# Kernel optimization log

Measured on AMD Instinct MI355X. Metric: run time of the kernel, lower is better.

The kernel has to match this reference:

```python
import jax, jax.numpy as jnp
import numpy as np

B, IN_C, OUT_C, NUM, DIM = 4096, 512, 512, 16, 128

def _unif(k, shape, fan_in):
    b = 1.0 / np.sqrt(fan_in)
    return jax.random.uniform(k, shape, jnp.float32, -b, b)

def setup_inputs() -> dict:
    key = jax.random.key(0)
    ks = jax.random.split(key, 9)
    inp = jax.random.normal(ks[0], (B, IN_C), jnp.float32)
    Wpre = _unif(ks[1], (DIM, IN_C), IN_C)        # nn.Linear weight (out, in)
    bpre = _unif(ks[2], (DIM,), IN_C)
    W = _unif(ks[3], (NUM, NUM, DIM, DIM), DIM)    # W[i,j] = link[i][j].weight (out=e, in=d)
    bl = _unif(ks[4], (NUM, NUM, DIM), DIM)        # link biases
    life = jax.random.uniform(ks[5], (NUM, NUM), jnp.float32) + 0.5  # rand(1)+0.5
    Wpost = _unif(ks[6], (OUT_C, DIM), DIM)
    bpost = _unif(ks[7], (OUT_C,), DIM)
    return {"inp": inp, "Wpre": Wpre, "bpre": bpre, "W": W, "b": bl,
            "life": life, "Wpost": Wpost, "bpost": bpost, "steps": 10}

def reference(inp, Wpre, bpre, W, b, life, Wpost, bpost, steps):
    num = life.shape[0]
    x = inp @ Wpre.T + bpre                         # [B, dim]
    gate = jnp.where(life > 0, life, 0.0)           # life>0 branch with scalar gain
    Wg = gate[:, :, None, None] * W                 # [num, num, dim, dim]
    bias = jnp.einsum('ij,ijd->jd', gate, b)        # per-step constant bias sum over i
    m0 = jnp.zeros((num,) + x.shape, x.dtype).at[0].set(x)  # matrix[0] = inp
    def step(m, _):
        # new[j] = sum_i gate[i,j] * (m[i] @ W[i,j].T + b[i,j])
        new = jnp.einsum('ibd,ijed->jbe', m, Wg) + bias[:, None, :]
        return new, None
    mT, _ = jax.lax.scan(step, m0, None, length=steps)
    return mT[num - 1] @ Wpost.T + bpost            # [B, out_c]
```

## Files before the change

kernel.cpp:

```cpp
#include <hip/hip_runtime.h>


typedef __bf16 bf16x8 __attribute__((ext_vector_type(8)));
typedef float f32x4 __attribute__((ext_vector_type(4)));
typedef __attribute__((address_space(3))) unsigned int lds_u32;
typedef const __attribute__((address_space(1))) unsigned int glb_u32;

__device__ __forceinline__ unsigned short f2bf(float x) {
  unsigned int u = __float_as_uint(x);
  u += 0x7FFFu + ((u >> 16) & 1u);
  return (unsigned short)(u >> 16);
}
__device__ __forceinline__ float bf2f(unsigned short s) {
  return __uint_as_float(((unsigned int)s) << 16);
}
__device__ __forceinline__ bf16x8 ldg8(const unsigned short* p) {
  return __builtin_bit_cast(bf16x8, *(const uint4*)p);
}
__device__ __forceinline__ f32x4 mfma16(bf16x8 a, bf16x8 b, f32x4 c) {
  return __builtin_amdgcn_mfma_f32_16x16x32_bf16(a, b, c, 0, 0, 0);
}

#define ND 2048
#define MT 144
#define KS 4
#define CKS 16

__global__ __launch_bounds__(256) void build_all(
    const float* __restrict__ W, const float* __restrict__ life,
    const float* __restrict__ bl, const float* __restrict__ inp,
    const float* __restrict__ Wpre, const float* __restrict__ Wpost,
    unsigned short* __restrict__ Ahi, unsigned short* __restrict__ Alo,
    unsigned short* __restrict__ AThi, unsigned short* __restrict__ ATlo,
    unsigned short* __restrict__ Qhi, unsigned short* __restrict__ Qlo,
    unsigned short* __restrict__ Rhi, unsigned short* __restrict__ Rlo,
    float* __restrict__ beta,
    unsigned short* __restrict__ Ihi, unsigned short* __restrict__ Ilo,
    unsigned short* __restrict__ Wph, unsigned short* __restrict__ Wpl,
    unsigned short* __restrict__ Woh, unsigned short* __restrict__ Wol,
    float* __restrict__ St, float* __restrict__ gv) {
  __shared__ unsigned short Th[32][36], Tl[32][36];
  const int tid = blockIdx.x * 256 + threadIdx.x;
  const int NT = gridDim.x * 256;
  const int t = threadIdx.x;

  {
    const int r = t >> 3;
    const int c4 = (t & 7) * 4;
    for (int tt = blockIdx.x; tt < 4096; tt += gridDim.x) {
      int nt = tt & 63, kt = tt >> 6;
      int j = nt >> 2, e0 = (nt & 3) * 32;
      int i = kt >> 2, d0 = (kt & 3) * 32;
      float gval = life[i * 16 + j];
      float gate = gval > 0.f ? gval : 0.f;
      const float* src = W + ((size_t)(i * 16 + j) * 16384 + (e0 + r) * 128 + d0 + c4);
      float4 v = *(const float4*)src;
      float vals[4] = {v.x, v.y, v.z, v.w};
      union { unsigned short u[4]; uint2 d2; } oh, ol;
#pragma unroll
      for (int x = 0; x < 4; ++x) {
        float s = gate * vals[x];
        oh.u[x] = f2bf(s);
        ol.u[x] = f2bf(s - bf2f(oh.u[x]));
      }
      size_t aidx = (size_t)(j * 128 + e0 + r) * ND + i * 128 + d0 + c4;
      *(uint2*)(Ahi + aidx) = oh.d2;
      *(uint2*)(Alo + aidx) = ol.d2;
      __syncthreads();
#pragma unroll
      for (int x = 0; x < 4; ++x) { Th[r][c4 + x] = oh.u[x]; Tl[r][c4 + x] = ol.u[x]; }
      __syncthreads();
      union { unsigned short u[4]; uint2 d2; } th, tl;
#pragma unroll
      for (int x = 0; x < 4; ++x) { th.u[x] = Th[c4 + x][r]; tl.u[x] = Tl[c4 + x][r]; }
      size_t tidx = (size_t)(i * 128 + d0 + r) * ND + j * 128 + e0 + c4;
      *(uint2*)(AThi + tidx) = th.d2;
      *(uint2*)(ATlo + tidx) = tl.d2;
    }
  }

  for (int item = tid; item < MT * ND; item += NT) {
    int m = item >> 11, n = item & 2047;
    int j = n >> 7, e = n & 127;
    unsigned short hh = 0, ll = 0;
    if (m < 128) {
      float gval = life[j];
      float gate = gval > 0.f ? gval : 0.f;
      float v = gate * W[j * 16384 + e * 128 + m];
      hh = f2bf(v); ll = f2bf(v - bf2f(hh));
    } else if (m == 128) {
      float s = 0.f;
#pragma unroll
      for (int i = 0; i < 16; ++i) {
        float gval = life[i * 16 + j];
        float gate = gval > 0.f ? gval : 0.f;
        s += gate * bl[(i * 16 + j) * 128 + e];
      }
      beta[n] = s;
      hh = f2bf(s); ll = f2bf(s - bf2f(hh));
    }
    Qhi[item] = hh;
    Qlo[item] = ll;
  }

  for (int item = tid; item < MT * ND; item += NT) {
    int m = item >> 11, n = item & 2047;
    int i = n >> 7, d = n & 127;
    unsigned short hh = 0, ll = 0;
    if (m < 128) {
      float gval = life[i * 16 + 15];
      float gate = gval > 0.f ? gval : 0.f;
      float v = gate * W[(size_t)(i * 16 + 15) * 16384 + m * 128 + d];
      hh = f2bf(v); ll = f2bf(v - bf2f(hh));
    }
    Rhi[item] = hh;
    Rlo[item] = ll;
  }

  for (int item = tid; item < (4096 * 512) / 8; item += NT) {
    int base = item * 8;
    float4 x = *(const float4*)(inp + base), y = *(const float4*)(inp + base + 4);
    float vals[8] = {x.x, x.y, x.z, x.w, y.x, y.y, y.z, y.w};
    union { unsigned short u[8]; uint4 v; } ph, pl;
#pragma unroll
    for (int q = 0; q < 8; ++q) {
      unsigned short h = f2bf(vals[q]);
      ph.u[q] = h;
      pl.u[q] = f2bf(vals[q] - bf2f(h));
    }
    *(uint4*)(Ihi + base) = ph.v;
    *(uint4*)(Ilo + base) = pl.v;
  }

  for (int item = tid; item < 16384; item += NT) {
    const float* src = (item < 8192) ? Wpre : Wpost;
    unsigned short* dh = (item < 8192) ? Wph : Woh;
    unsigned short* dl = (item < 8192) ? Wpl : Wol;
    int base = (item < 8192 ? item : item - 8192) * 8;
    float4 x = *(const float4*)(src + base), y = *(const float4*)(src + base + 4);
    float vals[8] = {x.x, x.y, x.z, x.w, y.x, y.y, y.z, y.w};
    union { unsigned short u[8]; uint4 v; } ph, pl;
#pragma unroll
    for (int q = 0; q < 8; ++q) {
      unsigned short h = f2bf(vals[q]);
      ph.u[q] = h;
      pl.u[q] = f2bf(vals[q] - bf2f(h));
    }
    *(uint4*)(dh + base) = ph.v;
    *(uint4*)(dl + base) = pl.v;
  }

  for (int item = tid; item < 4128; item += NT) {
    float4 z = {0.f, 0.f, 0.f, 0.f};
    if (item < 4096) *(float4*)(St + item * 4) = z;
    else             *(float4*)(gv + (item - 4096) * 4) = z;
  }
}

__global__ __launch_bounds__(192, 2) void step_pair(
    const unsigned short* __restrict__ Ahi, const unsigned short* __restrict__ Alo,
    const unsigned short* __restrict__ AThi, const unsigned short* __restrict__ ATlo,
    const unsigned short* __restrict__ Qqhi, const unsigned short* __restrict__ Qqlo,
    const unsigned short* __restrict__ Qrhi, const unsigned short* __restrict__ Qrlo,
    float* __restrict__ Pq, float* __restrict__ Pr) {
  __shared__ __align__(16) unsigned short AS[2][64][256];
  const int t = threadIdx.x;
  const int g = t >> 6, lane = t & 63;
  const int r16 = lane & 15, q = lane >> 4;
  const int kc = blockIdx.x;
  const int nb = blockIdx.y;
  const int chain = blockIdx.z;
  const unsigned short* Bh = chain ? AThi : Ahi;
  const unsigned short* Bl = chain ? ATlo : Alo;
  const unsigned short* Qh = chain ? Qrhi : Qqhi;
  const unsigned short* Ql = chain ? Qrlo : Qqlo;
  float* P = chain ? Pr : Pq;
  const int kbase = kc * 512;
  const int n0 = nb * 32;

  for (int ch = g; ch < 64; ch += 3) {
    int half = ch >> 5, c2 = ch & 31;
    int s = c2 * 64 + lane;
    int row = s >> 5;
    int c16 = (s & 31) ^ (row & 7);
    const unsigned short* src =
        (row < 32 ? Bh + (size_t)(n0 + row) * ND
                  : Bl + (size_t)(n0 + row - 32) * ND) + kbase + half * 256 + c16 * 8;
    __builtin_amdgcn_global_load_lds((glb_u32*)src,
                                     (lds_u32*)(&AS[0][0][0] + ch * 512), 16, 0, 0);
  }

  const int m0 = g * 48 + r16;
  const unsigned short* pA0h = Qh + (size_t)m0 * ND + kbase + q * 8;
  const unsigned short* pA0l = Ql + (size_t)m0 * ND + kbase + q * 8;

  bf16x8 qa[2][6];
#pragma unroll
  for (int f = 0; f < 3; ++f) {
    qa[0][2 * f]     = ldg8(pA0h + f * 16 * ND);
    qa[0][2 * f + 1] = ldg8(pA0l + f * 16 * ND);
  }
  __syncthreads();

  const uint4* ASv = (const uint4*)&AS[0][0][0];

  f32x4 acc[3][2];
#pragma unroll
  for (int mt = 0; mt < 3; ++mt)
#pragma unroll
    for (int nt = 0; nt < 2; ++nt) acc[mt][nt] = (f32x4){0.f, 0.f, 0.f, 0.f};

#pragma unroll
  for (int it = 0; it < 16; ++it) {
    const int cur = it & 1, nxt = cur ^ 1;
    if (it < 15) {
      const int ko = (it + 1) * 32;
#pragma unroll
      for (int f = 0; f < 3; ++f) {
        qa[nxt][2 * f]     = ldg8(pA0h + f * 16 * ND + ko);
        qa[nxt][2 * f + 1] = ldg8(pA0l + f * 16 * ND + ko);
      }
    }
    const int hbase = (it >> 3) * 2048;
    const int it8 = it & 7;
    const int cx = (it8 * 4 + q) ^ (r16 & 7);
    bf16x8 b0h = __builtin_bit_cast(bf16x8, ASv[hbase + r16 * 32 + cx]);
    bf16x8 b1h = __builtin_bit_cast(bf16x8, ASv[hbase + (16 + r16) * 32 + cx]);
    bf16x8 b0l = __builtin_bit_cast(bf16x8, ASv[hbase + (32 + r16) * 32 + cx]);
    bf16x8 b1l = __builtin_bit_cast(bf16x8, ASv[hbase + (48 + r16) * 32 + cx]);

    acc[0][0] = mfma16(qa[cur][0], b0h, acc[0][0]);
    acc[0][0] = mfma16(qa[cur][1], b0h, acc[0][0]);
    acc[0][0] = mfma16(qa[cur][0], b0l, acc[0][0]);
    acc[1][0] = mfma16(qa[cur][2], b0h, acc[1][0]);
    acc[1][0] = mfma16(qa[cur][3], b0h, acc[1][0]);
    acc[1][0] = mfma16(qa[cur][2], b0l, acc[1][0]);
    acc[2][0] = mfma16(qa[cur][4], b0h, acc[2][0]);
    acc[2][0] = mfma16(qa[cur][5], b0h, acc[2][0]);
    acc[2][0] = mfma16(qa[cur][4], b0l, acc[2][0]);
    acc[0][1] = mfma16(qa[cur][0], b1h, acc[0][1]);
    acc[0][1] = mfma16(qa[cur][1], b1h, acc[0][1]);
    acc[0][1] = mfma16(qa[cur][0], b1l, acc[0][1]);
    acc[1][1] = mfma16(qa[cur][2], b1h, acc[1][1]);
    acc[1][1] = mfma16(qa[cur][3], b1h, acc[1][1]);
    acc[1][1] = mfma16(qa[cur][2], b1l, acc[1][1]);
    acc[2][1] = mfma16(qa[cur][4], b1h, acc[2][1]);
    acc[2][1] = mfma16(qa[cur][5], b1h, acc[2][1]);
    acc[2][1] = mfma16(qa[cur][4], b1l, acc[2][1]);
  }

  float* Pk = P + kc * (MT * ND);
#pragma unroll
  for (int mt = 0; mt < 3; ++mt)
#pragma unroll
    for (int nt = 0; nt < 2; ++nt) {
      int mbase = g * 48 + mt * 16 + q * 4;
      int n = n0 + nt * 16 + r16;
#pragma unroll
      for (int r = 0; r < 4; ++r)
        Pk[(mbase + r) * ND + n] = acc[mt][nt][r];
    }
}

__global__ __launch_bounds__(256) void reduce_pair(
    const float* __restrict__ Pq, const float* __restrict__ Pr,
    const float* __restrict__ beta,
    unsigned short* __restrict__ Oqh, unsigned short* __restrict__ Oql,
    unsigned short* __restrict__ Orh, unsigned short* __restrict__ Orl) {
  int bid = blockIdx.x;
  int chain = bid >= 288;
  int t = (bid - (chain ? 288 : 0)) * 256 + threadIdx.x;
  const float* P = chain ? Pr : Pq;
  unsigned short* Oh = chain ? Orh : Oqh;
  unsigned short* Ol = chain ? Orl : Oql;
  int m = t >> 9;
  int n = (t & 511) * 4;
  int idx = m * ND + n;
  const int stride = MT * ND;
  float v0 = 0.f, v1 = 0.f, v2 = 0.f, v3 = 0.f;
#pragma unroll
  for (int c = 0; c < KS; ++c) {
    float4 s = *(const float4*)(P + c * stride + idx);
    v0 += s.x; v1 += s.y; v2 += s.z; v3 += s.w;
  }
  if (!chain && m == 128) {
    float4 b4 = *(const float4*)(beta + n);
    v0 += b4.x; v1 += b4.y; v2 += b4.z; v3 += b4.w;
  }
  union { unsigned short u[4]; uint2 d; } h, l;
  float vv[4] = {v0, v1, v2, v3};
#pragma unroll
  for (int i = 0; i < 4; ++i) {
    unsigned short hh = f2bf(vv[i]);
    h.u[i] = hh;
    l.u[i] = f2bf(vv[i] - bf2f(hh));
  }
  *(uint2*)(Oh + idx) = h.d;
  *(uint2*)(Ol + idx) = l.d;
}

__global__ __launch_bounds__(192, 2) void contract_S(
    const unsigned short* __restrict__ R5h, const unsigned short* __restrict__ R5l,
    const unsigned short* __restrict__ Q5h, const unsigned short* __restrict__ Q5l,
    float* __restrict__ St, float* __restrict__ gv) {
  __shared__ __align__(16) unsigned short AS[64][128];
  const int t = threadIdx.x;
  const int g = t >> 6, lane = t & 63;
  const int r16 = lane & 15, q = lane >> 4;
  const int kc = blockIdx.x;
  const int nb = blockIdx.y;
  const int kbase = kc * 128;
  const int n0 = nb * 32;

  for (int ch = g; ch < 16; ch += 3) {
    int s = ch * 64 + lane;
    int row = s >> 4;
    int c16 = (s & 15) ^ (row & 7);
    const unsigned short* src =
        (row < 32 ? R5h + (size_t)(n0 + row) * ND
                  : R5l + (size_t)(n0 + row - 32) * ND) + kbase + c16 * 8;
    __builtin_amdgcn_global_load_lds((glb_u32*)src,
                                     (lds_u32*)(&AS[0][0] + ch * 512), 16, 0, 0);
  }

  const int m0 = g * 48 + r16;
  const unsigned short* pA0h = Q5h + (size_t)m0 * ND + kbase + q * 8;
  const unsigned short* pA0l = Q5l + (size_t)m0 * ND + kbase + q * 8;

  bf16x8 qa[2][6];
#pragma unroll
  for (int f = 0; f < 3; ++f) {
    qa[0][2 * f]     = ldg8(pA0h + f * 16 * ND);
    qa[0][2 * f + 1] = ldg8(pA0l + f * 16 * ND);
  }
  __syncthreads();

  const uint4* ASv = (const uint4*)&AS[0][0];

  f32x4 acc[3][2];
#pragma unroll
  for (int mt = 0; mt < 3; ++mt)
#pragma unroll
    for (int nt = 0; nt < 2; ++nt) acc[mt][nt] = (f32x4){0.f, 0.f, 0.f, 0.f};

#pragma unroll
  for (int it = 0; it < 4; ++it) {
    const int cur = it & 1, nxt = cur ^ 1;
    if (it < 3) {
      const int ko = (it + 1) * 32;
#pragma unroll
      for (int f = 0; f < 3; ++f) {
        qa[nxt][2 * f]     = ldg8(pA0h + f * 16 * ND + ko);
        qa[nxt][2 * f + 1] = ldg8(pA0l + f * 16 * ND + ko);
      }
    }
    const int cx = (it * 4 + q) ^ (r16 & 7);
    bf16x8 b0h = __builtin_bit_cast(bf16x8, ASv[r16 * 16 + cx]);
    bf16x8 b1h = __builtin_bit_cast(bf16x8, ASv[(16 + r16) * 16 + cx]);
    bf16x8 b0l = __builtin_bit_cast(bf16x8, ASv[(32 + r16) * 16 + cx]);
    bf16x8 b1l = __builtin_bit_cast(bf16x8, ASv[(48 + r16) * 16 + cx]);

    acc[0][0] = mfma16(qa[cur][0], b0h, acc[0][0]);
    acc[0][0] = mfma16(qa[cur][1], b0h, acc[0][0]);
    acc[0][0] = mfma16(qa[cur][0], b0l, acc[0][0]);
    acc[1][0] = mfma16(qa[cur][2], b0h, acc[1][0]);
    acc[1][0] = mfma16(qa[cur][3], b0h, acc[1][0]);
    acc[1][0] = mfma16(qa[cur][2], b0l, acc[1][0]);
    acc[2][0] = mfma16(qa[cur][4], b0h, acc[2][0]);
    acc[2][0] = mfma16(qa[cur][5], b0h, acc[2][0]);
    acc[2][0] = mfma16(qa[cur][4], b0l, acc[2][0]);
    acc[0][1] = mfma16(qa[cur][0], b1h, acc[0][1]);
    acc[0][1] = mfma16(qa[cur][1], b1h, acc[0][1]);
    acc[0][1] = mfma16(qa[cur][0], b1l, acc[0][1]);
    acc[1][1] = mfma16(qa[cur][2], b1h, acc[1][1]);
    acc[1][1] = mfma16(qa[cur][3], b1h, acc[1][1]);
    acc[1][1] = mfma16(qa[cur][2], b1l, acc[1][1]);
    acc[2][1] = mfma16(qa[cur][4], b1h, acc[2][1]);
    acc[2][1] = mfma16(qa[cur][5], b1h, acc[2][1]);
    acc[2][1] = mfma16(qa[cur][4], b1l, acc[2][1]);
  }

#pragma unroll
  for (int mt = 0; mt < 3; ++mt)
#pragma unroll
    for (int nt = 0; nt < 2; ++nt) {
      int mbase = g * 48 + mt * 16 + q * 4;
      int n = n0 + nt * 16 + r16;
#pragma unroll
      for (int r = 0; r < 4; ++r) {
        int m = mbase + r;
        if (m < 128)       atomicAdd(St + m * 128 + n, acc[mt][nt][r]);
        else if (m == 128) atomicAdd(gv + n, acc[mt][nt][r]);
      }
    }
}

__global__ __launch_bounds__(256) void tail_small(
    const float* __restrict__ St, const float* __restrict__ gv,
    const unsigned short* __restrict__ Q5h, const unsigned short* __restrict__ Q5l,
    const float* __restrict__ bpre, const float* __restrict__ Wpost,
    const float* __restrict__ bpost,
    unsigned short* __restrict__ Seh, unsigned short* __restrict__ Sel,
    float* __restrict__ beff) {
  const int t = threadIdx.x;
  if (blockIdx.x == 0) {
    __shared__ float gl[128];
    if (t < 128) {
      int idx = 128 * ND + 1920 + t;
      float s = gv[t] + bf2f(Q5h[idx]) + bf2f(Q5l[idx]);
      for (int d = 0; d < 128; ++d) s += St[d * 128 + t] * bpre[d];
      gl[t] = s;
    }
    __syncthreads();
    for (int o = t; o < 512; o += 256) {
      float s = bpost[o];
      for (int e = 0; e < 128; ++e) s += Wpost[o * 128 + e] * gl[e];
      beff[o] = s;
    }
  } else {
    int base = (blockIdx.x - 1) * 1024 + t * 4;
    int e = base >> 7, d0 = base & 127;
    union { unsigned short u[4]; uint2 d2; } h, l;
#pragma unroll
    for (int i = 0; i < 4; ++i) {
      float v = St[(d0 + i) * 128 + e];
      h.u[i] = f2bf(v);
      l.u[i] = f2bf(v - bf2f(h.u[i]));
    }
    *(uint2*)(Seh + base) = h.d2;
    *(uint2*)(Sel + base) = l.d2;
  }
}

__global__ __launch_bounds__(256) void gemm_X1(
    const unsigned short* __restrict__ Ihi, const unsigned short* __restrict__ Ilo,
    const unsigned short* __restrict__ Wph, const unsigned short* __restrict__ Wpl,
    unsigned short* __restrict__ X1h, unsigned short* __restrict__ X1l) {
  __shared__ __align__(16) unsigned short Is_hi[64][40], Is_lo[64][40];
  __shared__ __align__(16) unsigned short Ws_hi[128][40], Ws_lo[128][40];
  const int t = threadIdx.x;
  const int mb = blockIdx.x;
  const int w = t >> 6, lane = t & 63;
  const int r16 = lane & 15, q = lane >> 4;

  f32x4 acc[4][2];
#pragma unroll
  for (int x = 0; x < 4; ++x)
#pragma unroll
    for (int b = 0; b < 2; ++b) acc[x][b] = (f32x4){0.f, 0.f, 0.f, 0.f};

  for (int kc = 0; kc < 16; ++kc) {
    const int k0 = kc * 32;
#pragma unroll
    for (int rpt = 0; rpt < 6; ++rpt) {
      int slot = t + rpt * 256;
      if (slot < 512) {
        int arr = slot >> 8, s = slot & 255;
        int row = s >> 2, off = (s & 3) * 8;
        const unsigned short* src = arr ? Ilo : Ihi;
        unsigned short* dst = arr ? &Is_lo[row][off] : &Is_hi[row][off];
        *(uint4*)dst = *(const uint4*)(src + (mb * 64 + row) * 512 + k0 + off);
      } else {
        int s = slot - 512;
        int arr = s >> 9, s2 = s & 511;
        int row = s2 >> 2, off = (s2 & 3) * 8;
        const unsigned short* src = arr ? Wpl : Wph;
        unsigned short* dst = arr ? &Ws_lo[row][off] : &Ws_hi[row][off];
        *(uint4*)dst = *(const uint4*)(src + row * 512 + k0 + off);
      }
    }
    __syncthreads();

    bf16x8 bh0 = __builtin_bit_cast(bf16x8, *(const uint4*)&Ws_hi[w * 32 + r16][q * 8]);
    bf16x8 bl0 = __builtin_bit_cast(bf16x8, *(const uint4*)&Ws_lo[w * 32 + r16][q * 8]);
    bf16x8 bh1 = __builtin_bit_cast(bf16x8, *(const uint4*)&Ws_hi[w * 32 + 16 + r16][q * 8]);
    bf16x8 bl1 = __builtin_bit_cast(bf16x8, *(const uint4*)&Ws_lo[w * 32 + 16 + r16][q * 8]);
#pragma unroll
    for (int mt = 0; mt < 4; ++mt) {
      bf16x8 ah = __builtin_bit_cast(bf16x8, *(const uint4*)&Is_hi[mt * 16 + r16][q * 8]);
      bf16x8 al = __builtin_bit_cast(bf16x8, *(const uint4*)&Is_lo[mt * 16 + r16][q * 8]);
      acc[mt][0] = mfma16(ah, bh0, acc[mt][0]);
      acc[mt][0] = mfma16(al, bh0, acc[mt][0]);
      acc[mt][0] = mfma16(ah, bl0, acc[mt][0]);
      acc[mt][1] = mfma16(ah, bh1, acc[mt][1]);
      acc[mt][1] = mfma16(al, bh1, acc[mt][1]);
      acc[mt][1] = mfma16(ah, bl1, acc[mt][1]);
    }
    __syncthreads();
  }

#pragma unroll
  for (int mt = 0; mt < 4; ++mt)
#pragma unroll
    for (int nt = 0; nt < 2; ++nt) {
      int n = w * 32 + nt * 16 + r16;
#pragma unroll
      for (int r = 0; r < 4; ++r) {
        int m = mb * 64 + mt * 16 + q * 4 + r;
        float v = acc[mt][nt][r];
        unsigned short h = f2bf(v);
        X1h[m * 128 + n] = h;
        X1l[m * 128 + n] = f2bf(v - bf2f(h));
      }
    }
}

__global__ __launch_bounds__(256) void gemm_X2(
    const unsigned short* __restrict__ X1h, const unsigned short* __restrict__ X1l,
    const unsigned short* __restrict__ Seh, const unsigned short* __restrict__ Sel,
    unsigned short* __restrict__ X2h, unsigned short* __restrict__ X2l) {
  __shared__ __align__(16) unsigned short Is_hi[64][40], Is_lo[64][40];
  __shared__ __align__(16) unsigned short Ws_hi[128][40], Ws_lo[128][40];
  const int t = threadIdx.x;
  const int mb = blockIdx.x;
  const int w = t >> 6, lane = t & 63;
  const int r16 = lane & 15, q = lane >> 4;

  f32x4 acc[4][2];
#pragma unroll
  for (int x = 0; x < 4; ++x)
#pragma unroll
    for (int b = 0; b < 2; ++b) acc[x][b] = (f32x4){0.f, 0.f, 0.f, 0.f};

  for (int kc = 0; kc < 4; ++kc) {
    const int k0 = kc * 32;
#pragma unroll
    for (int rpt = 0; rpt < 6; ++rpt) {
      int slot = t + rpt * 256;
      if (slot < 512) {
        int arr = slot >> 8, s = slot & 255;
        int row = s >> 2, off = (s & 3) * 8;
        const unsigned short* src = arr ? X1l : X1h;
        unsigned short* dst = arr ? &Is_lo[row][off] : &Is_hi[row][off];
        *(uint4*)dst = *(const uint4*)(src + (mb * 64 + row) * 128 + k0 + off);
      } else {
        int s = slot - 512;
        int arr = s >> 9, s2 = s & 511;
        int row = s2 >> 2, off = (s2 & 3) * 8;
        const unsigned short* src = arr ? Sel : Seh;
        unsigned short* dst = arr ? &Ws_lo[row][off] : &Ws_hi[row][off];
        *(uint4*)dst = *(const uint4*)(src + row * 128 + k0 + off);
      }
    }
    __syncthreads();

    bf16x8 bh0 = __builtin_bit_cast(bf16x8, *(const uint4*)&Ws_hi[w * 32 + r16][q * 8]);
    bf16x8 bl0 = __builtin_bit_cast(bf16x8, *(const uint4*)&Ws_lo[w * 32 + r16][q * 8]);
    bf16x8 bh1 = __builtin_bit_cast(bf16x8, *(const uint4*)&Ws_hi[w * 32 + 16 + r16][q * 8]);
    bf16x8 bl1 = __builtin_bit_cast(bf16x8, *(const uint4*)&Ws_lo[w * 32 + 16 + r16][q * 8]);
#pragma unroll
    for (int mt = 0; mt < 4; ++mt) {
      bf16x8 ah = __builtin_bit_cast(bf16x8, *(const uint4*)&Is_hi[mt * 16 + r16][q * 8]);
      bf16x8 al = __builtin_bit_cast(bf16x8, *(const uint4*)&Is_lo[mt * 16 + r16][q * 8]);
      acc[mt][0] = mfma16(ah, bh0, acc[mt][0]);
      acc[mt][0] = mfma16(al, bh0, acc[mt][0]);
      acc[mt][0] = mfma16(ah, bl0, acc[mt][0]);
      acc[mt][1] = mfma16(ah, bh1, acc[mt][1]);
      acc[mt][1] = mfma16(al, bh1, acc[mt][1]);
      acc[mt][1] = mfma16(ah, bl1, acc[mt][1]);
    }
    __syncthreads();
  }

#pragma unroll
  for (int mt = 0; mt < 4; ++mt)
#pragma unroll
    for (int nt = 0; nt < 2; ++nt) {
      int n = w * 32 + nt * 16 + r16;
#pragma unroll
      for (int r = 0; r < 4; ++r) {
        int m = mb * 64 + mt * 16 + q * 4 + r;
        float v = acc[mt][nt][r];
        unsigned short h = f2bf(v);
        X2h[m * 128 + n] = h;
        X2l[m * 128 + n] = f2bf(v - bf2f(h));
      }
    }
}

__global__ __launch_bounds__(256) void gemm_X3(
    const unsigned short* __restrict__ X2h, const unsigned short* __restrict__ X2l,
    const unsigned short* __restrict__ Woh, const unsigned short* __restrict__ Wol,
    const float* __restrict__ beff, float* __restrict__ out) {
  __shared__ __align__(16) unsigned short Is_hi[64][40], Is_lo[64][40];
  __shared__ __align__(16) unsigned short Ws_hi[128][40], Ws_lo[128][40];
  const int t = threadIdx.x;
  const int mb = blockIdx.x, nb = blockIdx.y;
  const int w = t >> 6, lane = t & 63;
  const int r16 = lane & 15, q = lane >> 4;

  f32x4 acc[4][2];
#pragma unroll
  for (int x = 0; x < 4; ++x)
#pragma unroll
    for (int b = 0; b < 2; ++b) acc[x][b] = (f32x4){0.f, 0.f, 0.f, 0.f};

  for (int kc = 0; kc < 4; ++kc) {
    const int k0 = kc * 32;
#pragma unroll
    for (int rpt = 0; rpt < 6; ++rpt) {
      int slot = t + rpt * 256;
      if (slot < 512) {
        int arr = slot >> 8, s = slot & 255;
        int row = s >> 2, off = (s & 3) * 8;
        const unsigned short* src = arr ? X2l : X2h;
        unsigned short* dst = arr ? &Is_lo[row][off] : &Is_hi[row][off];
        *(uint4*)dst = *(const uint4*)(src + (mb * 64 + row) * 128 + k0 + off);
      } else {
        int s = slot - 512;
        int arr = s >> 9, s2 = s & 511;
        int row = s2 >> 2, off = (s2 & 3) * 8;
        const unsigned short* src = arr ? Wol : Woh;
        unsigned short* dst = arr ? &Ws_lo[row][off] : &Ws_hi[row][off];
        *(uint4*)dst = *(const uint4*)(src + (nb * 128 + row) * 128 + k0 + off);
      }
    }
    __syncthreads();

    bf16x8 bh0 = __builtin_bit_cast(bf16x8, *(const uint4*)&Ws_hi[w * 32 + r16][q * 8]);
    bf16x8 bl0 = __builtin_bit_cast(bf16x8, *(const uint4*)&Ws_lo[w * 32 + r16][q * 8]);
    bf16x8 bh1 = __builtin_bit_cast(bf16x8, *(const uint4*)&Ws_hi[w * 32 + 16 + r16][q * 8]);
    bf16x8 bl1 = __builtin_bit_cast(bf16x8, *(const uint4*)&Ws_lo[w * 32 + 16 + r16][q * 8]);
#pragma unroll
    for (int mt = 0; mt < 4; ++mt) {
      bf16x8 ah = __builtin_bit_cast(bf16x8, *(const uint4*)&Is_hi[mt * 16 + r16][q * 8]);
      bf16x8 al = __builtin_bit_cast(bf16x8, *(const uint4*)&Is_lo[mt * 16 + r16][q * 8]);
      acc[mt][0] = mfma16(ah, bh0, acc[mt][0]);
      acc[mt][0] = mfma16(al, bh0, acc[mt][0]);
      acc[mt][0] = mfma16(ah, bl0, acc[mt][0]);
      acc[mt][1] = mfma16(ah, bh1, acc[mt][1]);
      acc[mt][1] = mfma16(al, bh1, acc[mt][1]);
      acc[mt][1] = mfma16(ah, bl1, acc[mt][1]);
    }
    __syncthreads();
  }

#pragma unroll
  for (int mt = 0; mt < 4; ++mt)
#pragma unroll
    for (int nt = 0; nt < 2; ++nt) {
      int n = nb * 128 + w * 32 + nt * 16 + r16;
      float bv = beff[n];
#pragma unroll
      for (int r = 0; r < 4; ++r) {
        int m = mb * 64 + mt * 16 + q * 4 + r;
        out[m * 512 + n] = acc[mt][nt][r] + bv;
      }
    }
}

extern "C" void kernel_launch(void* const* d_in, const int* in_sizes, int n_in,
                              void* d_out, int out_size, void* d_ws, size_t ws_size,
                              hipStream_t stream) {
  const float* inp   = (const float*)d_in[0];
  const float* Wpre  = (const float*)d_in[1];
  const float* bpre  = (const float*)d_in[2];
  const float* W     = (const float*)d_in[3];
  const float* bl    = (const float*)d_in[4];
  const float* life  = (const float*)d_in[5];
  const float* Wpost = (const float*)d_in[6];
  const float* bpost = (const float*)d_in[7];
  float* out = (float*)d_out;

  char* p = (char*)d_ws;
  auto alloc = [&](size_t bytes) {
    char* r = p;
    p += (bytes + 255) & ~(size_t)255;
    return r;
  };
  unsigned short* Ahi  = (unsigned short*)alloc((size_t)ND * ND * 2);
  unsigned short* Alo  = (unsigned short*)alloc((size_t)ND * ND * 2);
  unsigned short* AThi = (unsigned short*)alloc((size_t)ND * ND * 2);
  unsigned short* ATlo = (unsigned short*)alloc((size_t)ND * ND * 2);
  unsigned short* QqAh = (unsigned short*)alloc((size_t)MT * ND * 2);
  unsigned short* QqAl = (unsigned short*)alloc((size_t)MT * ND * 2);
  unsigned short* QqBh = (unsigned short*)alloc((size_t)MT * ND * 2);
  unsigned short* QqBl = (unsigned short*)alloc((size_t)MT * ND * 2);
  unsigned short* QrAh = (unsigned short*)alloc((size_t)MT * ND * 2);
  unsigned short* QrAl = (unsigned short*)alloc((size_t)MT * ND * 2);
  unsigned short* QrBh = (unsigned short*)alloc((size_t)MT * ND * 2);
  unsigned short* QrBl = (unsigned short*)alloc((size_t)MT * ND * 2);
  float* beta = (float*)alloc(ND * 4);
  float* Pq   = (float*)alloc((size_t)KS * MT * ND * 4);
  float* Pr   = (float*)alloc((size_t)KS * MT * ND * 4);
  float* St   = (float*)alloc(128 * 128 * 4);
  float* gv   = (float*)alloc(128 * 4);
  float* beff = (float*)alloc(512 * 4);
  unsigned short* Ihi = (unsigned short*)alloc((size_t)4096 * 512 * 2);
  unsigned short* Ilo = (unsigned short*)alloc((size_t)4096 * 512 * 2);
  unsigned short* Wph = (unsigned short*)alloc(128 * 512 * 2);
  unsigned short* Wpl = (unsigned short*)alloc(128 * 512 * 2);
  unsigned short* Woh = (unsigned short*)alloc(512 * 128 * 2);
  unsigned short* Wol = (unsigned short*)alloc(512 * 128 * 2);
  unsigned short* Seh = (unsigned short*)alloc(128 * 128 * 2);
  unsigned short* Sel = (unsigned short*)alloc(128 * 128 * 2);
  unsigned short* X1h = (unsigned short*)alloc((size_t)4096 * 128 * 2);
  unsigned short* X1l = (unsigned short*)alloc((size_t)4096 * 128 * 2);
  unsigned short* X2h = (unsigned short*)alloc((size_t)4096 * 128 * 2);
  unsigned short* X2l = (unsigned short*)alloc((size_t)4096 * 128 * 2);

  build_all<<<1024, 256, 0, stream>>>(W, life, bl, inp, Wpre, Wpost,
                                      Ahi, Alo, AThi, ATlo,
                                      QqAh, QqAl, QrAh, QrAl, beta, Ihi, Ilo,
                                      Wph, Wpl, Woh, Wol, St, gv);
  gemm_X1<<<dim3(64, 1), 256, 0, stream>>>(Ihi, Ilo, Wph, Wpl, X1h, X1l);

  const unsigned short *qqh = QqAh, *qql = QqAl, *qrh = QrAh, *qrl = QrAl;
  unsigned short *oqh = QqBh, *oql = QqBl, *orh = QrBh, *orl = QrBl;
  for (int s = 0; s < 4; ++s) {
    step_pair<<<dim3(KS, 64, 2), 192, 0, stream>>>(
        Ahi, Alo, AThi, ATlo, qqh, qql, qrh, qrl, Pq, Pr);
    reduce_pair<<<576, 256, 0, stream>>>(Pq, Pr, beta, oqh, oql, orh, orl);
    const unsigned short* t1 = qqh; qqh = oqh; oqh = (unsigned short*)t1;
    const unsigned short* t2 = qql; qql = oql; oql = (unsigned short*)t2;
    const unsigned short* t3 = qrh; qrh = orh; orh = (unsigned short*)t3;
    const unsigned short* t4 = qrl; qrl = orl; orl = (unsigned short*)t4;
  }

  contract_S<<<dim3(CKS, 4), 192, 0, stream>>>(qrh, qrl, qqh, qql, St, gv);
  tail_small<<<17, 256, 0, stream>>>(St, gv, qqh, qql, bpre, Wpost, bpost,
                                     Seh, Sel, beff);
  gemm_X2<<<dim3(64, 1), 256, 0, stream>>>(X1h, X1l, Seh, Sel, X2h, X2l);
  gemm_X3<<<dim3(64, 4), 256, 0, stream>>>(X2h, X2l, Woh, Wol, beff, out);
}
```

Before: 247.6 us.

## Fuse X1 GEMM into build kernel and merge tail GEMMs into one kernel

The input projection GEMM now runs inside the build kernel as 64 extra blocks. Those blocks convert inp and Wpre to hi/lo bf16 on the fly instead of staging them through global buffers. The tail_small, gemm_X2 and gemm_X3 kernels become one out_fused kernel. It computes the effective bias per block, converts the transposed S matrix directly from fp32, and keeps X2 in LDS before the output GEMM. This removes several launches and the global round trips for the I, X2 and S buffers, but every output block now recomputes the bias and the S conversion, and only 64 blocks are launched.

```diff
diff --git a/kernel.cpp b/kernel.cpp
--- a/kernel.cpp
+++ b/kernel.cpp
@@ -26,6 +26,26 @@
 #define KS 4
 #define CKS 16
 
+#define GEMM_MFMA(IsH, IsL, WsH, WsL)                                         \
+  {                                                                           \
+    bf16x8 bh0 = __builtin_bit_cast(bf16x8, *(const uint4*)&WsH[w * 32 + r16][q * 8]);      \
+    bf16x8 bl0 = __builtin_bit_cast(bf16x8, *(const uint4*)&WsL[w * 32 + r16][q * 8]);      \
+    bf16x8 bh1 = __builtin_bit_cast(bf16x8, *(const uint4*)&WsH[w * 32 + 16 + r16][q * 8]); \
+    bf16x8 bl1 = __builtin_bit_cast(bf16x8, *(const uint4*)&WsL[w * 32 + 16 + r16][q * 8]); \
+    _Pragma("unroll")                                                         \
+    for (int mt = 0; mt < 4; ++mt) {                                          \
+      bf16x8 ah = __builtin_bit_cast(bf16x8, *(const uint4*)&IsH[mt * 16 + r16][q * 8]);    \
+      bf16x8 al = __builtin_bit_cast(bf16x8, *(const uint4*)&IsL[mt * 16 + r16][q * 8]);    \
+      acc[mt][0] = mfma16(ah, bh0, acc[mt][0]);                               \
+      acc[mt][0] = mfma16(al, bh0, acc[mt][0]);                               \
+      acc[mt][0] = mfma16(ah, bl0, acc[mt][0]);                               \
+      acc[mt][1] = mfma16(ah, bh1, acc[mt][1]);                               \
+      acc[mt][1] = mfma16(al, bh1, acc[mt][1]);                               \
+      acc[mt][1] = mfma16(ah, bl1, acc[mt][1]);                               \
+    }                                                                         \
+  }
+
+#define BJOBS 960
 __global__ __launch_bounds__(256) void build_all(
     const float* __restrict__ W, const float* __restrict__ life,
     const float* __restrict__ bl, const float* __restrict__ inp,
@@ -35,19 +55,85 @@
     unsigned short* __restrict__ Qhi, unsigned short* __restrict__ Qlo,
     unsigned short* __restrict__ Rhi, unsigned short* __restrict__ Rlo,
     float* __restrict__ beta,
-    unsigned short* __restrict__ Ihi, unsigned short* __restrict__ Ilo,
-    unsigned short* __restrict__ Wph, unsigned short* __restrict__ Wpl,
     unsigned short* __restrict__ Woh, unsigned short* __restrict__ Wol,
-    float* __restrict__ St, float* __restrict__ gv) {
+    unsigned short* __restrict__ X1h, unsigned short* __restrict__ X1l,
+    float* __restrict__ Ste, float* __restrict__ gv) {
   __shared__ unsigned short Th[32][36], Tl[32][36];
-  const int tid = blockIdx.x * 256 + threadIdx.x;
-  const int NT = gridDim.x * 256;
+  __shared__ __align__(16) unsigned short IsH2[64][40], IsL2[64][40];
+  __shared__ __align__(16) unsigned short WsH2[128][40], WsL2[128][40];
   const int t = threadIdx.x;
+
+  if (blockIdx.x >= BJOBS) {
+    const int mb = blockIdx.x - BJOBS;
+    const int w = t >> 6, lane = t & 63;
+    const int r16 = lane & 15, q = lane >> 4;
+    f32x4 acc[4][2];
+#pragma unroll
+    for (int x = 0; x < 4; ++x)
+#pragma unroll
+      for (int b = 0; b < 2; ++b) acc[x][b] = (f32x4){0.f, 0.f, 0.f, 0.f};
+
+    for (int kc = 0; kc < 16; ++kc) {
+      const int k0 = kc * 32;
+#pragma unroll
+      for (int rpt = 0; rpt < 6; ++rpt) {
+        int slot = t + rpt * 256;
+        union { unsigned short u[8]; uint4 v; } pk;
+        if (slot < 512) {
+          int arr = slot >> 8, s = slot & 255;
+          int row = s >> 2, off = (s & 3) * 8;
+          const float* src = inp + (mb * 64 + row) * 512 + k0 + off;
+#pragma unroll
+          for (int i = 0; i < 8; ++i) {
+            float v = src[i];
+            unsigned short h = f2bf(v);
+            pk.u[i] = arr ? f2bf(v - bf2f(h)) : h;
+          }
+          unsigned short* dst = arr ? &IsL2[row][off] : &IsH2[row][off];
+          *(uint4*)dst = pk.v;
+        } else {
+          int s = slot - 512;
+          int arr = s >> 9, s2 = s & 511;
+          int row = s2 >> 2, off = (s2 & 3) * 8;
+          const float* src = Wpre + row * 512 + k0 + off;
+#pragma unroll
+          for (int i = 0; i < 8; ++i) {
+            float v = src[i];
+            unsigned short h = f2bf(v);
+            pk.u[i] = arr ? f2bf(v - bf2f(h)) : h;
+          }
+          unsigned short* dst = arr ? &WsL2[row][off] : &WsH2[row][off];
+          *(uint4*)dst = pk.v;
+        }
+      }
+      __syncthreads();
+      GEMM_MFMA(IsH2, IsL2, WsH2, WsL2)
+      __syncthreads();
+    }
+#pragma unroll
+    for (int mt = 0; mt < 4; ++mt)
+#pragma unroll
+      for (int nt = 0; nt < 2; ++nt) {
+        int n = w * 32 + nt * 16 + r16;
+#pragma unroll
+        for (int r = 0; r < 4; ++r) {
+          int m = mb * 64 + mt * 16 + q * 4 + r;
+          float v = acc[mt][nt][r];
+          unsigned short h = f2bf(v);
+          X1h[m * 128 + n] = h;
+          X1l[m * 128 + n] = f2bf(v - bf2f(h));
+        }
+      }
+    return;
+  }
+
+  const int tid = blockIdx.x * 256 + t;
+  const int NT = BJOBS * 256;
 
   {
     const int r = t >> 3;
     const int c4 = (t & 7) * 4;
-    for (int tt = blockIdx.x; tt < 4096; tt += gridDim.x) {
+    for (int tt = blockIdx.x; tt < 4096; tt += BJOBS) {
       int nt = tt & 63, kt = tt >> 6;
       int j = nt >> 2, e0 = (nt & 3) * 32;
       int i = kt >> 2, d0 = (kt & 3) * 32;
@@ -117,42 +203,24 @@
     Rlo[item] = ll;
   }
 
-  for (int item = tid; item < (4096 * 512) / 8; item += NT) {
+  for (int item = tid; item < 8192; item += NT) {
     int base = item * 8;
-    float4 x = *(const float4*)(inp + base), y = *(const float4*)(inp + base + 4);
+    float4 x = *(const float4*)(Wpost + base), y = *(const float4*)(Wpost + base + 4);
     float vals[8] = {x.x, x.y, x.z, x.w, y.x, y.y, y.z, y.w};
     union { unsigned short u[8]; uint4 v; } ph, pl;
 #pragma unroll
-    for (int q = 0; q < 8; ++q) {
-      unsigned short h = f2bf(vals[q]);
-      ph.u[q] = h;
-      pl.u[q] = f2bf(vals[q] - bf2f(h));
-    }
-    *(uint4*)(Ihi + base) = ph.v;
-    *(uint4*)(Ilo + base) = pl.v;
-  }
-
-  for (int item = tid; item < 16384; item += NT) {
-    const float* src = (item < 8192) ? Wpre : Wpost;
-    unsigned short* dh = (item < 8192) ? Wph : Woh;
-    unsigned short* dl = (item < 8192) ? Wpl : Wol;
-    int base = (item < 8192 ? item : item - 8192) * 8;
-    float4 x = *(const float4*)(src + base), y = *(const float4*)(src + base + 4);
-    float vals[8] = {x.x, x.y, x.z, x.w, y.x, y.y, y.z, y.w};
-    union { unsigned short u[8]; uint4 v; } ph, pl;
-#pragma unroll
-    for (int q = 0; q < 8; ++q) {
-      unsigned short h = f2bf(vals[q]);
-      ph.u[q] = h;
-      pl.u[q] = f2bf(vals[q] - bf2f(h));
-    }
-    *(uint4*)(dh + base) = ph.v;
-    *(uint4*)(dl + base) = pl.v;
+    for (int q2 = 0; q2 < 8; ++q2) {
+      unsigned short h = f2bf(vals[q2]);
+      ph.u[q2] = h;
+      pl.u[q2] = f2bf(vals[q2] - bf2f(h));
+    }
+    *(uint4*)(Woh + base) = ph.v;
+    *(uint4*)(Wol + base) = pl.v;
   }
 
   for (int item = tid; item < 4128; item += NT) {
     float4 z = {0.f, 0.f, 0.f, 0.f};
-    if (item < 4096) *(float4*)(St + item * 4) = z;
+    if (item < 4096) *(float4*)(Ste + item * 4) = z;
     else             *(float4*)(gv + (item - 4096) * 4) = z;
   }
 }
@@ -302,7 +370,7 @@
 __global__ __launch_bounds__(192, 2) void contract_S(
     const unsigned short* __restrict__ R5h, const unsigned short* __restrict__ R5l,
     const unsigned short* __restrict__ Q5h, const unsigned short* __restrict__ Q5l,
-    float* __restrict__ St, float* __restrict__ gv) {
+    float* __restrict__ Ste, float* __restrict__ gv) {
   __shared__ __align__(16) unsigned short AS[64][128];
   const int t = threadIdx.x;
   const int g = t >> 6, lane = t & 63;
@@ -389,132 +457,55 @@
 #pragma unroll
       for (int r = 0; r < 4; ++r) {
         int m = mbase + r;
-        if (m < 128)       atomicAdd(St + m * 128 + n, acc[mt][nt][r]);
+        if (m < 128)       atomicAdd(Ste + n * 128 + m, acc[mt][nt][r]);
         else if (m == 128) atomicAdd(gv + n, acc[mt][nt][r]);
       }
     }
 }
 
-__global__ __launch_bounds__(256) void tail_small(
-    const float* __restrict__ St, const float* __restrict__ gv,
+__global__ __launch_bounds__(256) void out_fused(
+    const unsigned short* __restrict__ X1h, const unsigned short* __restrict__ X1l,
+    const float* __restrict__ Ste, const float* __restrict__ gv,
     const unsigned short* __restrict__ Q5h, const unsigned short* __restrict__ Q5l,
     const float* __restrict__ bpre, const float* __restrict__ Wpost,
     const float* __restrict__ bpost,
-    unsigned short* __restrict__ Seh, unsigned short* __restrict__ Sel,
-    float* __restrict__ beff) {
-  const int t = threadIdx.x;
-  if (blockIdx.x == 0) {
-    __shared__ float gl[128];
-    if (t < 128) {
-      int idx = 128 * ND + 1920 + t;
-      float s = gv[t] + bf2f(Q5h[idx]) + bf2f(Q5l[idx]);
-      for (int d = 0; d < 128; ++d) s += St[d * 128 + t] * bpre[d];
-      gl[t] = s;
-    }
-    __syncthreads();
-    for (int o = t; o < 512; o += 256) {
-      float s = bpost[o];
-      for (int e = 0; e < 128; ++e) s += Wpost[o * 128 + e] * gl[e];
-      beff[o] = s;
-    }
-  } else {
-    int base = (blockIdx.x - 1) * 1024 + t * 4;
-    int e = base >> 7, d0 = base & 127;
-    union { unsigned short u[4]; uint2 d2; } h, l;
-#pragma unroll
-    for (int i = 0; i < 4; ++i) {
-      float v = St[(d0 + i) * 128 + e];
-      h.u[i] = f2bf(v);
-      l.u[i] = f2bf(v - bf2f(h.u[i]));
-    }
-    *(uint2*)(Seh + base) = h.d2;
-    *(uint2*)(Sel + base) = l.d2;
-  }
-}
-
-__global__ __launch_bounds__(256) void gemm_X1(
-    const unsigned short* __restrict__ Ihi, const unsigned short* __restrict__ Ilo,
-    const unsigned short* __restrict__ Wph, const unsigned short* __restrict__ Wpl,
-    unsigned short* __restrict__ X1h, unsigned short* __restrict__ X1l) {
-  __shared__ __align__(16) unsigned short Is_hi[64][40], Is_lo[64][40];
-  __shared__ __align__(16) unsigned short Ws_hi[128][40], Ws_lo[128][40];
+    const unsigned short* __restrict__ Woh, const unsigned short* __restrict__ Wol,
+    float* __restrict__ out) {
+  __shared__ __align__(16) char buf[65536];
+  unsigned short (*X2H)[136] = (unsigned short(*)[136])(buf);
+  unsigned short (*X2L)[136] = (unsigned short(*)[136])(buf + 17408);
+  unsigned short (*WsH)[40]  = (unsigned short(*)[40])(buf + 34816);
+  unsigned short (*WsL)[40]  = (unsigned short(*)[40])(buf + 45056);
+  unsigned short (*IsH)[40]  = (unsigned short(*)[40])(buf + 55296);
+  unsigned short (*IsL)[40]  = (unsigned short(*)[40])(buf + 60416);
+  float* gl    = (float*)(buf + 55296);
+  float* beffl = (float*)(buf + 34816);
+
   const int t = threadIdx.x;
   const int mb = blockIdx.x;
   const int w = t >> 6, lane = t & 63;
   const int r16 = lane & 15, q = lane >> 4;
 
-  f32x4 acc[4][2];
-#pragma unroll
-  for (int x = 0; x < 4; ++x)
-#pragma unroll
-    for (int b = 0; b < 2; ++b) acc[x][b] = (f32x4){0.f, 0.f, 0.f, 0.f};
-
-  for (int kc = 0; kc < 16; ++kc) {
-    const int k0 = kc * 32;
-#pragma unroll
-    for (int rpt = 0; rpt < 6; ++rpt) {
-      int slot = t + rpt * 256;
-      if (slot < 512) {
-        int arr = slot >> 8, s = slot & 255;
-        int row = s >> 2, off = (s & 3) * 8;
-        const unsigned short* src = arr ? Ilo : Ihi;
-        unsigned short* dst = arr ? &Is_lo[row][off] : &Is_hi[row][off];
-        *(uint4*)dst = *(const uint4*)(src + (mb * 64 + row) * 512 + k0 + off);
-      } else {
-        int s = slot - 512;
-        int arr = s >> 9, s2 = s & 511;
-        int row = s2 >> 2, off = (s2 & 3) * 8;
-        const unsigned short* src = arr ? Wpl : Wph;
-        unsigned short* dst = arr ? &Ws_lo[row][off] : &Ws_hi[row][off];
-        *(uint4*)dst = *(const uint4*)(src + row * 512 + k0 + off);
-      }
-    }
-    __syncthreads();
-
-    bf16x8 bh0 = __builtin_bit_cast(bf16x8, *(const uint4*)&Ws_hi[w * 32 + r16][q * 8]);
-    bf16x8 bl0 = __builtin_bit_cast(bf16x8, *(const uint4*)&Ws_lo[w * 32 + r16][q * 8]);
-    bf16x8 bh1 = __builtin_bit_cast(bf16x8, *(const uint4*)&Ws_hi[w * 32 + 16 + r16][q * 8]);
-    bf16x8 bl1 = __builtin_bit_cast(bf16x8, *(const uint4*)&Ws_lo[w * 32 + 16 + r16][q * 8]);
-#pragma unroll
-    for (int mt = 0; mt < 4; ++mt) {
-      bf16x8 ah = __builtin_bit_cast(bf16x8, *(const uint4*)&Is_hi[mt * 16 + r16][q * 8]);
-      bf16x8 al = __builtin_bit_cast(bf16x8, *(const uint4*)&Is_lo[mt * 16 + r16][q * 8]);
-      acc[mt][0] = mfma16(ah, bh0, acc[mt][0]);
-      acc[mt][0] = mfma16(al, bh0, acc[mt][0]);
-      acc[mt][0] = mfma16(ah, bl0, acc[mt][0]);
-      acc[mt][1] = mfma16(ah, bh1, acc[mt][1]);
-      acc[mt][1] = mfma16(al, bh1, acc[mt][1]);
-      acc[mt][1] = mfma16(ah, bl1, acc[mt][1]);
-    }
-    __syncthreads();
-  }
-
-#pragma unroll
-  for (int mt = 0; mt < 4; ++mt)
-#pragma unroll
-    for (int nt = 0; nt < 2; ++nt) {
-      int n = w * 32 + nt * 16 + r16;
-#pragma unroll
-      for (int r = 0; r < 4; ++r) {
-        int m = mb * 64 + mt * 16 + q * 4 + r;
-        float v = acc[mt][nt][r];
-        unsigned short h = f2bf(v);
-        X1h[m * 128 + n] = h;
-        X1l[m * 128 + n] = f2bf(v - bf2f(h));
-      }
-    }
-}
-
-__global__ __launch_bounds__(256) void gemm_X2(
-    const unsigned short* __restrict__ X1h, const unsigned short* __restrict__ X1l,
-    const unsigned short* __restrict__ Seh, const unsigned short* __restrict__ Sel,
-    unsigned short* __restrict__ X2h, unsigned short* __restrict__ X2l) {
-  __shared__ __align__(16) unsigned short Is_hi[64][40], Is_lo[64][40];
-  __shared__ __align__(16) unsigned short Ws_hi[128][40], Ws_lo[128][40];
-  const int t = threadIdx.x;
-  const int mb = blockIdx.x;
-  const int w = t >> 6, lane = t & 63;
-  const int r16 = lane & 15, q = lane >> 4;
+  if (t < 128) {
+    int idx = 128 * ND + 1920 + t;
+    float s = gv[t] + bf2f(Q5h[idx]) + bf2f(Q5l[idx]);
+    for (int d = 0; d < 128; ++d) s += Ste[t * 128 + d] * bpre[d];
+    gl[t] = s;
+  }
+  __syncthreads();
+  for (int o = t; o < 512; o += 256) {
+    float s = bpost[o];
+    for (int e = 0; e < 128; ++e) s += Wpost[o * 128 + e] * gl[e];
+    beffl[o] = s;
+  }
+  __syncthreads();
+  float bef[8];
+#pragma unroll
+  for (int nb2 = 0; nb2 < 4; ++nb2)
+#pragma unroll
+    for (int nt = 0; nt < 2; ++nt)
+      bef[nb2 * 2 + nt] = beffl[nb2 * 128 + w * 32 + nt * 16 + r16];
+  __syncthreads();
 
   f32x4 acc[4][2];
 #pragma unroll
@@ -531,122 +522,94 @@
         int arr = slot >> 8, s = slot & 255;
         int row = s >> 2, off = (s & 3) * 8;
         const unsigned short* src = arr ? X1l : X1h;
-        unsigned short* dst = arr ? &Is_lo[row][off] : &Is_hi[row][off];
+        unsigned short* dst = arr ? &IsL[row][off] : &IsH[row][off];
         *(uint4*)dst = *(const uint4*)(src + (mb * 64 + row) * 128 + k0 + off);
       } else {
         int s = slot - 512;
         int arr = s >> 9, s2 = s & 511;
         int row = s2 >> 2, off = (s2 & 3) * 8;
-        const unsigned short* src = arr ? Sel : Seh;
-        unsigned short* dst = arr ? &Ws_lo[row][off] : &Ws_hi[row][off];
-        *(uint4*)dst = *(const uint4*)(src + row * 128 + k0 + off);
+        const float* src = Ste + row * 128 + k0 + off;
+        union { unsigned short u[8]; uint4 v; } pk;
+#pragma unroll
+        for (int i = 0; i < 8; ++i) {
+          float v = src[i];
+          unsigned short h = f2bf(v);
+          pk.u[i] = arr ? f2bf(v - bf2f(h)) : h;
+        }
+        unsigned short* dst = arr ? &WsL[row][off] : &WsH[row][off];
+        *(uint4*)dst = pk.v;
       }
     }
     __syncthreads();
-
-    bf16x8 bh0 = __builtin_bit_cast(bf16x8, *(const uint4*)&Ws_hi[w * 32 + r16][q * 8]);
-    bf16x8 bl0 = __builtin_bit_cast(bf16x8, *(const uint4*)&Ws_lo[w * 32 + r16][q * 8]);
-    bf16x8 bh1 = __builtin_bit_cast(bf16x8, *(const uint4*)&Ws_hi[w * 32 + 16 + r16][q * 8]);
-    bf16x8 bl1 = __builtin_bit_cast(bf16x8, *(const uint4*)&Ws_lo[w * 32 + 16 + r16][q * 8]);
-#pragma unroll
-    for (int mt = 0; mt < 4; ++mt) {
-      bf16x8 ah = __builtin_bit_cast(bf16x8, *(const uint4*)&Is_hi[mt * 16 + r16][q * 8]);
-      bf16x8 al = __builtin_bit_cast(bf16x8, *(const uint4*)&Is_lo[mt * 16 + r16][q * 8]);
-      acc[mt][0] = mfma16(ah, bh0, acc[mt][0]);
-      acc[mt][0] = mfma16(al, bh0, acc[mt][0]);
-      acc[mt][0] = mfma16(ah, bl0, acc[mt][0]);
-      acc[mt][1] = mfma16(ah, bh1, acc[mt][1]);
-      acc[mt][1] = mfma16(al, bh1, acc[mt][1]);
-      acc[mt][1] = mfma16(ah, bl1, acc[mt][1]);
-    }
+    GEMM_MFMA(IsH, IsL, WsH, WsL)
     __syncthreads();
   }
-
 #pragma unroll
   for (int mt = 0; mt < 4; ++mt)
 #pragma unroll
     for (int nt = 0; nt < 2; ++nt) {
-      int n = w * 32 + nt * 16 + r16;
+      int col = w * 32 + nt * 16 + r16;
 #pragma unroll
       for (int r = 0; r < 4; ++r) {
-        int m = mb * 64 + mt * 16 + q * 4 + r;
+        int row = mt * 16 + q * 4 + r;
         float v = acc[mt][nt][r];
         unsigned short h = f2bf(v);
-        X2h[m * 128 + n] = h;
-        X2l[m * 128 + n] = f2bf(v - bf2f(h));
-      }
-    }
-}
-
-__global__ __launch_bounds__(256) void gemm_X3(
-    const unsigned short* __restrict__ X2h, const unsigned short* __restrict__ X2l,
-    const unsigned short* __restrict__ Woh, const unsigned short* __restrict__ Wol,
-    const float* __restrict__ beff, float* __restrict__ out) {
-  __shared__ __align__(16) unsigned short Is_hi[64][40], Is_lo[64][40];
-  __shared__ __align__(16) unsigned short Ws_hi[128][40], Ws_lo[128][40];
-  const int t = threadIdx.x;
-  const int mb = blockIdx.x, nb = blockIdx.y;
-  const int w = t >> 6, lane = t & 63;
-  const int r16 = lane & 15, q = lane >> 4;
-
-  f32x4 acc[4][2];
-#pragma unroll
-  for (int x = 0; x < 4; ++x)
-#pragma unroll
-    for (int b = 0; b < 2; ++b) acc[x][b] = (f32x4){0.f, 0.f, 0.f, 0.f};
-
-  for (int kc = 0; kc < 4; ++kc) {
-    const int k0 = kc * 32;
-#pragma unroll
-    for (int rpt = 0; rpt < 6; ++rpt) {
-      int slot = t + rpt * 256;
-      if (slot < 512) {
-        int arr = slot >> 8, s = slot & 255;
-        int row = s >> 2, off = (s & 3) * 8;
-        const unsigned short* src = arr ? X2l : X2h;
-        unsigned short* dst = arr ? &Is_lo[row][off] : &Is_hi[row][off];
-        *(uint4*)dst = *(const uint4*)(src + (mb * 64 + row) * 128 + k0 + off);
-      } else {
-        int s = slot - 512;
+        X2H[row][col] = h;
+        X2L[row][col] = f2bf(v - bf2f(h));
+      }
+    }
+  __syncthreads();
+
+#pragma unroll 1
+  for (int nb2 = 0; nb2 < 4; ++nb2) {
+    f32x4 acc3[4][2];
+#pragma unroll
+    for (int x = 0; x < 4; ++x)
+#pragma unroll
+      for (int b = 0; b < 2; ++b) acc3[x][b] = (f32x4){0.f, 0.f, 0.f, 0.f};
+
+    for (int kc = 0; kc < 4; ++kc) {
+      const int k0 = kc * 32;
+#pragma unroll
+      for (int rpt = 0; rpt < 4; ++rpt) {
+        int s = t + rpt * 256;
         int arr = s >> 9, s2 = s & 511;
         int row = s2 >> 2, off = (s2 & 3) * 8;
         const unsigned short* src = arr ? Wol : Woh;
-        unsigned short* dst = arr ? &Ws_lo[row][off] : &Ws_hi[row][off];
-        *(uint4*)dst = *(const uint4*)(src + (nb * 128 + row) * 128 + k0 + off);
-      }
-    }
-    __syncthreads();
-
-    bf16x8 bh0 = __builtin_bit_cast(bf16x8, *(const uint4*)&Ws_hi[w * 32 + r16][q * 8]);
-    bf16x8 bl0 = __builtin_bit_cast(bf16x8, *(const uint4*)&Ws_lo[w * 32 + r16][q * 8]);
-    bf16x8 bh1 = __builtin_bit_cast(bf16x8, *(const uint4*)&Ws_hi[w * 32 + 16 + r16][q * 8]);
-    bf16x8 bl1 = __builtin_bit_cast(bf16x8, *(const uint4*)&Ws_lo[w * 32 + 16 + r16][q * 8]);
-#pragma unroll
-    for (int mt = 0; mt < 4; ++mt) {
-      bf16x8 ah = __builtin_bit_cast(bf16x8, *(const uint4*)&Is_hi[mt * 16 + r16][q * 8]);
-      bf16x8 al = __builtin_bit_cast(bf16x8, *(const uint4*)&Is_lo[mt * 16 + r16][q * 8]);
-      acc[mt][0] = mfma16(ah, bh0, acc[mt][0]);
-      acc[mt][0] = mfma16(al, bh0, acc[mt][0]);
-      acc[mt][0] = mfma16(ah, bl0, acc[mt][0]);
-      acc[mt][1] = mfma16(ah, bh1, acc[mt][1]);
-      acc[mt][1] = mfma16(al, bh1, acc[mt][1]);
-      acc[mt][1] = mfma16(ah, bl1, acc[mt][1]);
-    }
-    __syncthreads();
-  }
-
-#pragma unroll
-  for (int mt = 0; mt < 4; ++mt)
-#pragma unroll
-    for (int nt = 0; nt < 2; ++nt) {
-      int n = nb * 128 + w * 32 + nt * 16 + r16;
-      float bv = beff[n];
-#pragma unroll
-      for (int r = 0; r < 4; ++r) {
-        int m = mb * 64 + mt * 16 + q * 4 + r;
-        out[m * 512 + n] = acc[mt][nt][r] + bv;
-      }
-    }
+        unsigned short* dst = arr ? &WsL[row][off] : &WsH[row][off];
+        *(uint4*)dst = *(const uint4*)(src + (nb2 * 128 + row) * 128 + k0 + off);
+      }
+      __syncthreads();
+      bf16x8 bh0 = __builtin_bit_cast(bf16x8, *(const uint4*)&WsH[w * 32 + r16][q * 8]);
+      bf16x8 bl0 = __builtin_bit_cast(bf16x8, *(const uint4*)&WsL[w * 32 + r16][q * 8]);
+      bf16x8 bh1 = __builtin_bit_cast(bf16x8, *(const uint4*)&WsH[w * 32 + 16 + r16][q * 8]);
+      bf16x8 bl1 = __builtin_bit_cast(bf16x8, *(const uint4*)&WsL[w * 32 + 16 + r16][q * 8]);
+#pragma unroll
+      for (int mt = 0; mt < 4; ++mt) {
+        bf16x8 ah = __builtin_bit_cast(bf16x8, *(const uint4*)&X2H[mt * 16 + r16][k0 + q * 8]);
+        bf16x8 al = __builtin_bit_cast(bf16x8, *(const uint4*)&X2L[mt * 16 + r16][k0 + q * 8]);
+        acc3[mt][0] = mfma16(ah, bh0, acc3[mt][0]);
+        acc3[mt][0] = mfma16(al, bh0, acc3[mt][0]);
+        acc3[mt][0] = mfma16(ah, bl0, acc3[mt][0]);
+        acc3[mt][1] = mfma16(ah, bh1, acc3[mt][1]);
+        acc3[mt][1] = mfma16(al, bh1, acc3[mt][1]);
+        acc3[mt][1] = mfma16(ah, bl1, acc3[mt][1]);
+      }
+      __syncthreads();
+    }
+#pragma unroll
+    for (int mt = 0; mt < 4; ++mt)
+#pragma unroll
+      for (int nt = 0; nt < 2; ++nt) {
+        int n = nb2 * 128 + w * 32 + nt * 16 + r16;
+        float bv = bef[nb2 * 2 + nt];
+#pragma unroll
+        for (int r = 0; r < 4; ++r) {
+          int m = mb * 64 + mt * 16 + q * 4 + r;
+          out[m * 512 + n] = acc3[mt][nt][r] + bv;
+        }
+      }
+  }
 }
 
 extern "C" void kernel_launch(void* const* d_in, const int* in_sizes, int n_in,
@@ -683,27 +646,17 @@
   float* beta = (float*)alloc(ND * 4);
   float* Pq   = (float*)alloc((size_t)KS * MT * ND * 4);
   float* Pr   = (float*)alloc((size_t)KS * MT * ND * 4);
-  float* St   = (float*)alloc(128 * 128 * 4);
+  float* Ste  = (float*)alloc(128 * 128 * 4);
   float* gv   = (float*)alloc(128 * 4);
-  float* beff = (float*)alloc(512 * 4);
-  unsigned short* Ihi = (unsigned short*)alloc((size_t)4096 * 512 * 2);
-  unsigned short* Ilo = (unsigned short*)alloc((size_t)4096 * 512 * 2);
-  unsigned short* Wph = (unsigned short*)alloc(128 * 512 * 2);
-  unsigned short* Wpl = (unsigned short*)alloc(128 * 512 * 2);
   unsigned short* Woh = (unsigned short*)alloc(512 * 128 * 2);
   unsigned short* Wol = (unsigned short*)alloc(512 * 128 * 2);
-  unsigned short* Seh = (unsigned short*)alloc(128 * 128 * 2);
-  unsigned short* Sel = (unsigned short*)alloc(128 * 128 * 2);
   unsigned short* X1h = (unsigned short*)alloc((size_t)4096 * 128 * 2);
   unsigned short* X1l = (unsigned short*)alloc((size_t)4096 * 128 * 2);
-  unsigned short* X2h = (unsigned short*)alloc((size_t)4096 * 128 * 2);
-  unsigned short* X2l = (unsigned short*)alloc((size_t)4096 * 128 * 2);
 
   build_all<<<1024, 256, 0, stream>>>(W, life, bl, inp, Wpre, Wpost,
                                       Ahi, Alo, AThi, ATlo,
-                                      QqAh, QqAl, QrAh, QrAl, beta, Ihi, Ilo,
-                                      Wph, Wpl, Woh, Wol, St, gv);
-  gemm_X1<<<dim3(64, 1), 256, 0, stream>>>(Ihi, Ilo, Wph, Wpl, X1h, X1l);
+                                      QqAh, QqAl, QrAh, QrAl, beta,
+                                      Woh, Wol, X1h, X1l, Ste, gv);
 
   const unsigned short *qqh = QqAh, *qql = QqAl, *qrh = QrAh, *qrl = QrAl;
   unsigned short *oqh = QqBh, *oql = QqBl, *orh = QrBh, *orl = QrBl;
@@ -717,9 +670,7 @@
     const unsigned short* t4 = qrl; qrl = orl; orl = (unsigned short*)t4;
   }
 
-  contract_S<<<dim3(CKS, 4), 192, 0, stream>>>(qrh, qrl, qqh, qql, St, gv);
-  tail_small<<<17, 256, 0, stream>>>(St, gv, qqh, qql, bpre, Wpost, bpost,
-                                     Seh, Sel, beff);
-  gemm_X2<<<dim3(64, 1), 256, 0, stream>>>(X1h, X1l, Seh, Sel, X2h, X2l);
-  gemm_X3<<<dim3(64, 4), 256, 0, stream>>>(X2h, X2l, Woh, Wol, beff, out);
-}
+  contract_S<<<dim3(CKS, 4), 192, 0, stream>>>(qrh, qrl, qqh, qql, Ste, gv);
+  out_fused<<<64, 256, 0, stream>>>(X1h, X1l, Ste, gv, qqh, qql,
+                                    bpre, Wpost, bpost, Woh, Wol, out);
+}
```

Measured after the change: 305.7 us. +23.5%, slower.
